# Performance work log

Hardware: AMD Instinct MI355X
Metric: run time of the kernel (lower is better)

The kernel has to match this reference:

```python
import jax, jax.numpy as jnp
import numpy as np

N_USERS = 1_000_000
AVG_DEG = 32
E = N_USERS * AVG_DEG
K = 5
IN_F = 1
OUT_F = 64
BN_EPS = 1e-5


def setup_inputs() -> dict:
    key = jax.random.key(0)
    ks = jax.random.split(key, 6)
    stdv = 1.0 / np.sqrt(IN_F * K)
    return {
        "x": jax.random.normal(ks[0], (N_USERS, IN_F), dtype=jnp.float32),
        "edge_index": jax.random.randint(ks[1], (2, E), 0, N_USERS, dtype=jnp.int32),
        "edge_weight": jax.random.uniform(ks[2], (E,), dtype=jnp.float32),
        "weight": jax.random.uniform(ks[3], (OUT_F, K, IN_F), dtype=jnp.float32, minval=-stdv, maxval=stdv),
        "bias": jax.random.uniform(ks[4], (OUT_F,), dtype=jnp.float32, minval=-stdv, maxval=stdv),
        "gamma": jnp.ones((N_USERS,), dtype=jnp.float32),
        "beta": jnp.zeros((N_USERS,), dtype=jnp.float32),
    }


def reference(x, edge_index, edge_weight, weight, bias, gamma, beta):
    N = x.shape[0]
    src, dst = edge_index[0], edge_index[1]
    # K-hop propagation: gather x_j, scale by edge_weight, scatter-add at dst
    feats = [x]
    cur = x
    for _ in range(K - 1):
        msg = cur[src] * edge_weight[:, None]                 # [E, IN_F]
        cur = jax.ops.segment_sum(msg, dst, num_segments=N)   # [N, IN_F]
        feats.append(cur)
    # [N, K*IN_F], hop-major / feature-minor ordering (matches torch reshape)
    conv = jnp.concatenate(feats, axis=1)[None]               # [1, N, K*IN_F]
    h = weight.reshape(OUT_F, K * IN_F).T                     # [K*IN_F, OUT_F]
    y = jnp.matmul(conv, h) + bias                            # [1, N, OUT_F]
    # BatchNorm1d(N_users) in training mode: stats over (batch, feature) per node-channel
    mean = jnp.mean(y, axis=(0, 2), keepdims=True)
    var = jnp.mean((y - mean) ** 2, axis=(0, 2), keepdims=True)  # biased var
    y_hat = (y - mean) * jax.lax.rsqrt(var + BN_EPS)
    return y_hat * gamma[None, :, None] + beta[None, :, None]
```

## Files before the change

### kernel.cpp

```cpp
#include <hip/hip_runtime.h>

#define N_USERS 1000000
#define NEDGE   32000000
#define OUT_F   64
#define BN_EPS  1e-5f

#define SBITS     12
#define S_BUCKET  4096
#define NB        245
#define CAP       136896
#define SCAT_BLOCKS 1024
#define TILE      4096
#define NTILES    ((NEDGE + TILE - 1) / TILE)
#define SPLIT     16

typedef unsigned int uint4v __attribute__((ext_vector_type(4)));
typedef int          int4v  __attribute__((ext_vector_type(4)));
typedef float        flt4v  __attribute__((ext_vector_type(4)));


__global__ void init_cursors(unsigned* __restrict__ cursors) {
    int i = blockIdx.x * blockDim.x + threadIdx.x;
    if (i < NB) cursors[i] = (unsigned)i * CAP;
}

__global__ __launch_bounds__(256) void scatter_bin(
    const int* __restrict__ src, const int* __restrict__ dst,
    const float* __restrict__ ew, uint2* __restrict__ rec,
    unsigned* __restrict__ cursors) {
    __shared__ uint2 srec[TILE];
    __shared__ unsigned short sbkt[TILE];
    __shared__ unsigned hist[NB];
    __shared__ unsigned curs[NB];
    __shared__ unsigned gpos[NB];
    __shared__ unsigned chunkT[256];
    int tid = threadIdx.x;

    for (int tile = blockIdx.x; tile < NTILES; tile += gridDim.x) {
        int e0 = tile * TILE;
        int n_this = (e0 + TILE <= NEDGE) ? TILE : (NEDGE - e0);
        int nq = n_this >> 2;
        int q0 = e0 >> 2;

        for (int i = tid; i < NB; i += 256) hist[i] = 0;
        __syncthreads();

        int4v dv[4]; int4v sv[4]; flt4v wv[4];
        #pragma unroll
        for (int k = 0; k < 4; ++k) {
            int q = k * 256 + tid;
            if (q < nq) {
                dv[k] = __builtin_nontemporal_load(reinterpret_cast<const int4v*>(dst) + q0 + q);
                sv[k] = __builtin_nontemporal_load(reinterpret_cast<const int4v*>(src) + q0 + q);
                wv[k] = __builtin_nontemporal_load(reinterpret_cast<const flt4v*>(ew) + q0 + q);
            }
        }
        #pragma unroll
        for (int k = 0; k < 4; ++k) {
            int q = k * 256 + tid;
            if (q < nq) {
                #pragma unroll
                for (int j = 0; j < 4; ++j)
                    atomicAdd(&hist[dv[k][j] >> SBITS], 1u);
            }
        }
        __syncthreads();

        {
            int base = tid * 4;
            unsigned run = 0;
            #pragma unroll
            for (int k = 0; k < 4; ++k) {
                int idx = base + k;
                unsigned v = (idx < NB) ? hist[idx] : 0u;
                if (idx < NB) hist[idx] = run;
                run += v;
            }
            chunkT[tid] = run;
        }
        __syncthreads();
        if (tid == 0) {
            unsigned r = 0;
            for (int t = 0; t < 256; ++t) { unsigned v = chunkT[t]; chunkT[t] = r; r += v; }
        }
        __syncthreads();
        {
            int base = tid * 4;
            unsigned add = chunkT[tid];
            #pragma unroll
            for (int k = 0; k < 4; ++k) {
                int idx = base + k;
                if (idx < NB) hist[idx] += add;
            }
        }
        __syncthreads();

        for (int b = tid; b < NB; b += 256) {
            unsigned st = hist[b];
            unsigned en = (b == NB - 1) ? (unsigned)n_this : hist[b + 1];
            unsigned c = en - st;
            gpos[b] = c ? atomicAdd(&cursors[b], c) : 0u;
            curs[b] = 0;
        }
        __syncthreads();

        #pragma unroll
        for (int k = 0; k < 4; ++k) {
            int q = k * 256 + tid;
            if (q < nq) {
                #pragma unroll
                for (int j = 0; j < 4; ++j) {
                    int dd = dv[k][j], ss = sv[k][j];
                    int b = dd >> SBITS;
                    unsigned p = hist[b] + atomicAdd(&curs[b], 1u);
                    srec[p] = make_uint2(((unsigned)(dd & (S_BUCKET - 1)) << 20) | (unsigned)ss,
                                         __float_as_uint(wv[k][j]));
                    sbkt[p] = (unsigned short)b;
                }
            }
        }
        __syncthreads();

        for (int i = tid; i < n_this; i += 256) {
            unsigned b = sbkt[i];
            rec[gpos[b] + ((unsigned)i - hist[b])] = srec[i];
        }
        __syncthreads();
    }
}

__global__ __launch_bounds__(256) void hop_bucket(
    const uint2* __restrict__ rec, const unsigned* __restrict__ cursors,
    const float* __restrict__ cur, float* __restrict__ nxt) {
    __shared__ float acc[S_BUCKET];
    int tid = threadIdx.x;
    int b = blockIdx.x / SPLIT;
    int sidx = blockIdx.x % SPLIT;
    for (int i = tid; i < S_BUCKET; i += 256) acc[i] = 0.0f;
    __syncthreads();

    unsigned start = (unsigned)b * CAP;
    unsigned cnt = cursors[b] - start;
    unsigned u0 = ((cnt * (unsigned)sidx) / SPLIT) & ~15u;
    unsigned u1 = (sidx == SPLIT - 1) ? cnt : (((cnt * (unsigned)(sidx + 1)) / SPLIT) & ~15u);
    const uint2* bp = rec + start;

    unsigned i = u0 + 16u * (unsigned)tid;
    for (; i + 16u <= u1; i += 16u * 256u) {
        uint4v r[8];
        #pragma unroll
        for (int k = 0; k < 8; ++k)
            r[k] = __builtin_nontemporal_load(reinterpret_cast<const uint4v*>(bp + i + 2 * k));
        float c[16];
        #pragma unroll
        for (int k = 0; k < 8; ++k) {
            c[2 * k]     = cur[r[k].x & 0xFFFFFu];
            c[2 * k + 1] = cur[r[k].z & 0xFFFFFu];
        }
        #pragma unroll
        for (int k = 0; k < 8; ++k) {
            atomicAdd(&acc[r[k].x >> 20], c[2 * k]     * __uint_as_float(r[k].y));
            atomicAdd(&acc[r[k].z >> 20], c[2 * k + 1] * __uint_as_float(r[k].w));
        }
    }
    if (i < u1) {
        for (unsigned j = i; j < i + 16u && j < u1; ++j) {
            uint2 rr = bp[j];
            atomicAdd(&acc[rr.x >> 20], cur[rr.x & 0xFFFFFu] * __uint_as_float(rr.y));
        }
    }
    __syncthreads();

    int nb0 = b << SBITS;
    for (int k = tid; k < S_BUCKET; k += 256) {
        int n = nb0 + k;
        if (n < N_USERS) atomicAdd(&nxt[n], acc[k]);
    }
}


__global__ void zero_kernel(float* __restrict__ p, int n) {
    int i = blockIdx.x * blockDim.x + threadIdx.x;
    int stride = gridDim.x * blockDim.x;
    for (; i < n; i += stride) p[i] = 0.0f;
}

__global__ __launch_bounds__(256) void hop_atomic(
    const int* __restrict__ src, const int* __restrict__ dst,
    const float* __restrict__ ew, const float* __restrict__ cur,
    float* __restrict__ nxt) {
    int e = blockIdx.x * blockDim.x + threadIdx.x;
    if (e * 4 < NEDGE) {
        int4   s = ((const int4*)src)[e];
        int4   d = ((const int4*)dst)[e];
        float4 w = ((const float4*)ew)[e];
        atomicAdd(&nxt[d.x], cur[s.x] * w.x);
        atomicAdd(&nxt[d.y], cur[s.y] * w.y);
        atomicAdd(&nxt[d.z], cur[s.z] * w.z);
        atomicAdd(&nxt[d.w], cur[s.w] * w.w);
    }
}


__global__ __launch_bounds__(256) void finalize_kernel(
    const float* __restrict__ x,  const float* __restrict__ f1,
    const float* __restrict__ f2, const float* __restrict__ f3,
    const float* __restrict__ f4, const float* __restrict__ W,
    const float* __restrict__ bias, const float* __restrict__ gamma,
    const float* __restrict__ beta, float* __restrict__ out) {
    int lane = threadIdx.x & 63;
    int waveInBlock = threadIdx.x >> 6;
    int wavesPerBlock = blockDim.x >> 6;
    int gwave  = blockIdx.x * wavesPerBlock + waveInBlock;
    int nwaves = gridDim.x * wavesPerBlock;

    float w0 = W[lane * 5 + 0];
    float w1 = W[lane * 5 + 1];
    float w2 = W[lane * 5 + 2];
    float w3 = W[lane * 5 + 3];
    float w4 = W[lane * 5 + 4];
    float b  = bias[lane];

    for (int n = gwave; n < N_USERS; n += nwaves) {
        float c0 = x[n], c1 = f1[n], c2 = f2[n], c3 = f3[n], c4 = f4[n];
        float y = b + c0 * w0 + c1 * w1 + c2 * w2 + c3 * w3 + c4 * w4;

        float s = y;
        #pragma unroll
        for (int off = 32; off; off >>= 1) s += __shfl_xor(s, off);
        float mean = s * (1.0f / 64.0f);

        float d = y - mean;
        float v = d * d;
        #pragma unroll
        for (int off = 32; off; off >>= 1) v += __shfl_xor(v, off);
        float var = v * (1.0f / 64.0f);

        float o = d * rsqrtf(var + BN_EPS) * gamma[n] + beta[n];
        __builtin_nontemporal_store(o, &out[(size_t)n * OUT_F + lane]);
    }
}

extern "C" void kernel_launch(void* const* d_in, const int* in_sizes, int n_in,
                              void* d_out, int out_size, void* d_ws, size_t ws_size,
                              hipStream_t stream) {
    const float* x     = (const float*)d_in[0];
    const int*   ei    = (const int*)d_in[1];
    const float* ew    = (const float*)d_in[2];
    const float* W     = (const float*)d_in[3];
    const float* bias  = (const float*)d_in[4];
    const float* gamma = (const float*)d_in[5];
    const float* beta  = (const float*)d_in[6];
    float* out = (float*)d_out;

    const int* src = ei;
    const int* dst = ei + NEDGE;

    float* f = (float*)d_ws;
    uint2* rec = (uint2*)(f + 4ull * N_USERS);
    unsigned* cursors = (unsigned*)(rec + (size_t)NB * CAP);
    size_t needed = 16000000ull + (size_t)NB * CAP * 8 + 4096;

    if (ws_size >= needed) {
        init_cursors<<<1, 256, 0, stream>>>(cursors);
        zero_kernel<<<2048, 256, 0, stream>>>(f, 4 * N_USERS);
        scatter_bin<<<SCAT_BLOCKS, 256, 0, stream>>>(src, dst, ew, rec, cursors);
        const float* cur = x;
        for (int h = 0; h < 4; ++h) {
            float* nxt = f + (size_t)h * N_USERS;
            hop_bucket<<<NB * SPLIT, 256, 0, stream>>>(rec, cursors, cur, nxt);
            cur = nxt;
        }
    } else {
        zero_kernel<<<4096, 256, 0, stream>>>(f, 4 * N_USERS);
        const float* cur = x;
        for (int h = 0; h < 4; ++h) {
            float* nxt = f + (size_t)h * N_USERS;
            hop_atomic<<<NEDGE / 4 / 256, 256, 0, stream>>>(src, dst, ew, cur, nxt);
            cur = nxt;
        }
    }

    finalize_kernel<<<2048, 256, 0, stream>>>(
        x, f, f + N_USERS, f + 2 * N_USERS, f + 3 * N_USERS,
        W, bias, gamma, beta, out);
}
```

Before: 1.859 ms.

## Regroup edges into dst-super/src-window bins and stage source windows in LDS

After: 3.555 ms. +91.2%, slower.

```diff
diff --git a/kernel.cpp b/kernel.cpp
--- a/kernel.cpp
+++ b/kernel.cpp
@@ -12,9 +12,21 @@
 #define SCAT_BLOCKS 1024
 #define TILE      4096
 #define NTILES    ((NEDGE + TILE - 1) / TILE)
-#define SPLIT     16
+
+#define SUP_B     6
+#define NSUP      41
+#define S_SUPER   24576
+#define NWIN      245
+#define NBINS2    (NSUP * NWIN)
+#define HSPLIT    6
+#define RGRID     1024
+
+static_assert((unsigned long long)NEDGE * 8ull ==
+              (unsigned long long)N_USERS * OUT_F * 4ull,
+              "compact rec2 must exactly fit d_out");
 
 typedef unsigned int uint4v __attribute__((ext_vector_type(4)));
+typedef unsigned int uint2v __attribute__((ext_vector_type(2)));
 typedef int          int4v  __attribute__((ext_vector_type(4)));
 typedef float        flt4v  __attribute__((ext_vector_type(4)));
 
@@ -129,52 +141,209 @@
     }
 }
 
-__global__ __launch_bounds__(256) void hop_bucket(
+
+__global__ __launch_bounds__(256) void count_bins(
     const uint2* __restrict__ rec, const unsigned* __restrict__ cursors,
+    unsigned* __restrict__ cnt2) {
+    __shared__ unsigned hist[NWIN];
+    int tid = threadIdx.x;
+    int b = blockIdx.x >> 2, q = blockIdx.x & 3;
+    for (int i = tid; i < NWIN; i += 256) hist[i] = 0;
+    __syncthreads();
+    unsigned cnt = cursors[b] - (unsigned)b * CAP;
+    unsigned lo = (unsigned)(((unsigned long long)cnt * (unsigned)q) >> 2);
+    unsigned hi = (q == 3) ? cnt : (unsigned)(((unsigned long long)cnt * (unsigned)(q + 1)) >> 2);
+    const uint2v* bp = reinterpret_cast<const uint2v*>(rec + (size_t)b * CAP);
+    unsigned i = lo + (unsigned)tid;
+    for (; i + 768 < hi; i += 1024) {
+        uint2v r0 = __builtin_nontemporal_load(bp + i);
+        uint2v r1 = __builtin_nontemporal_load(bp + i + 256);
+        uint2v r2 = __builtin_nontemporal_load(bp + i + 512);
+        uint2v r3 = __builtin_nontemporal_load(bp + i + 768);
+        atomicAdd(&hist[(r0.x & 0xFFFFFu) >> 12], 1u);
+        atomicAdd(&hist[(r1.x & 0xFFFFFu) >> 12], 1u);
+        atomicAdd(&hist[(r2.x & 0xFFFFFu) >> 12], 1u);
+        atomicAdd(&hist[(r3.x & 0xFFFFFu) >> 12], 1u);
+    }
+    for (; i < hi; i += 256) {
+        uint2v r = __builtin_nontemporal_load(bp + i);
+        atomicAdd(&hist[(r.x & 0xFFFFFu) >> 12], 1u);
+    }
+    __syncthreads();
+    unsigned base = (unsigned)(b / SUP_B) * (unsigned)NWIN;
+    for (int k = tid; k < NWIN; k += 256)
+        if (hist[k]) atomicAdd(&cnt2[base + k], hist[k]);
+}
+
+
+__global__ __launch_bounds__(256) void prefix_bins(
+    const unsigned* __restrict__ cnt2, unsigned* __restrict__ bases,
+    unsigned* __restrict__ cursors2) {
+    __shared__ unsigned chunkT[256];
+    int t = threadIdx.x;
+    unsigned loc[40];
+    unsigned run = 0;
+    for (int k = 0; k < 40; ++k) {
+        int idx = t * 40 + k;
+        unsigned v = (idx < NBINS2) ? cnt2[idx] : 0u;
+        loc[k] = run; run += v;
+    }
+    chunkT[t] = run;
+    __syncthreads();
+    if (t == 0) {
+        unsigned r = 0;
+        for (int i = 0; i < 256; ++i) { unsigned v = chunkT[i]; chunkT[i] = r; r += v; }
+    }
+    __syncthreads();
+    unsigned add = chunkT[t];
+    for (int k = 0; k < 40; ++k) {
+        int idx = t * 40 + k;
+        if (idx < NBINS2) { unsigned v = loc[k] + add; bases[idx] = v; cursors2[idx] = v; }
+    }
+    if (t == 0) bases[NBINS2] = (unsigned)NEDGE;
+}
+
+
+__global__ __launch_bounds__(256) void regroup(
+    const uint2* __restrict__ rec, const unsigned* __restrict__ cursors,
+    uint2* __restrict__ rec2, unsigned* __restrict__ cursors2) {
+    __shared__ uint2 srec[TILE];
+    __shared__ unsigned char skey[TILE];
+    __shared__ unsigned hist[NWIN];
+    __shared__ unsigned curs[NWIN];
+    __shared__ unsigned gpos[NWIN];
+    __shared__ unsigned chunkT[256];
+    int tid = threadIdx.x;
+
+    for (int b = 0; b < NB; ++b) {
+        unsigned cntb = cursors[b] - (unsigned)b * CAP;
+        unsigned binbase = (unsigned)(b / SUP_B) * (unsigned)NWIN;
+        unsigned rb = (unsigned)(b % SUP_B) << 12;
+        int ntiles = (int)((cntb + TILE - 1) / TILE);
+        const uint2* bp = rec + (size_t)b * CAP;
+
+        for (int t = blockIdx.x; t < ntiles; t += gridDim.x) {
+            unsigned e0 = (unsigned)t * TILE;
+            unsigned n_this = (cntb - e0 < TILE) ? (cntb - e0) : TILE;
+
+            for (int i = tid; i < NWIN; i += 256) hist[i] = 0;
+            __syncthreads();
+
+            uint4v rv[8];
+            #pragma unroll
+            for (int k2 = 0; k2 < 8; ++k2) {
+                unsigned idx = (unsigned)(k2 * 512 + tid * 2);
+                if (idx < n_this)
+                    rv[k2] = __builtin_nontemporal_load(
+                        reinterpret_cast<const uint4v*>(bp + e0 + idx));
+            }
+            #pragma unroll
+            for (int k2 = 0; k2 < 8; ++k2) {
+                unsigned idx = (unsigned)(k2 * 512 + tid * 2);
+                if (idx < n_this)     atomicAdd(&hist[(rv[k2].x & 0xFFFFFu) >> 12], 1u);
+                if (idx + 1 < n_this) atomicAdd(&hist[(rv[k2].z & 0xFFFFFu) >> 12], 1u);
+            }
+            __syncthreads();
+
+            chunkT[tid] = (tid < NWIN) ? hist[tid] : 0u;
+            __syncthreads();
+            if (tid == 0) {
+                unsigned r = 0;
+                for (int i = 0; i < 256; ++i) { unsigned v = chunkT[i]; chunkT[i] = r; r += v; }
+            }
+            __syncthreads();
+            if (tid < NWIN) hist[tid] = chunkT[tid];
+            __syncthreads();
+            if (tid < NWIN) {
+                unsigned st = hist[tid];
+                unsigned en = (tid == NWIN - 1) ? n_this : hist[tid + 1];
+                unsigned c = en - st;
+                gpos[tid] = c ? atomicAdd(&cursors2[binbase + tid], c) : 0u;
+                curs[tid] = 0;
+            }
+            __syncthreads();
+
+            #pragma unroll
+            for (int k2 = 0; k2 < 8; ++k2) {
+                unsigned idx = (unsigned)(k2 * 512 + tid * 2);
+                if (idx < n_this) {
+                    unsigned m = rv[k2].x;
+                    unsigned k = (m & 0xFFFFFu) >> 12;
+                    unsigned p = hist[k] + atomicAdd(&curs[k], 1u);
+                    srec[p] = make_uint2((((m >> 20) + rb) << 12) | (m & 0xFFFu), rv[k2].y);
+                    skey[p] = (unsigned char)k;
+                }
+                if (idx + 1 < n_this) {
+                    unsigned m = rv[k2].z;
+                    unsigned k = (m & 0xFFFFFu) >> 12;
+                    unsigned p = hist[k] + atomicAdd(&curs[k], 1u);
+                    srec[p] = make_uint2((((m >> 20) + rb) << 12) | (m & 0xFFFu), rv[k2].w);
+                    skey[p] = (unsigned char)k;
+                }
+            }
+            __syncthreads();
+
+            for (unsigned i = (unsigned)tid; i < n_this; i += 256) {
+                unsigned k = skey[i];
+                rec2[gpos[k] + (i - hist[k])] = srec[i];
+            }
+            __syncthreads();
+        }
+    }
+}
+
+
+__global__ __launch_bounds__(512) void hop_super(
+    const uint2* __restrict__ rec2, const unsigned* __restrict__ bases,
     const float* __restrict__ cur, float* __restrict__ nxt) {
-    __shared__ float acc[S_BUCKET];
+    __shared__ float acc[S_SUPER];
+    __shared__ float win[4096];
     int tid = threadIdx.x;
-    int b = blockIdx.x / SPLIT;
-    int sidx = blockIdx.x % SPLIT;
-    for (int i = tid; i < S_BUCKET; i += 256) acc[i] = 0.0f;
+    int s = blockIdx.x / HSPLIT;
+    int j = blockIdx.x % HSPLIT;
+    for (int i = tid; i < S_SUPER; i += 512) acc[i] = 0.0f;
+
+    for (int k = j; k < NWIN; k += HSPLIT) {
+        __syncthreads();
+        int wbase = k << 12;
+        for (int i = tid; i < 4096; i += 512) {
+            int g = wbase + i;
+            win[i] = (g < N_USERS) ? cur[g] : 0.0f;
+        }
+        __syncthreads();
+
+        unsigned lo = bases[s * NWIN + k];
+        unsigned hi = bases[s * NWIN + k + 1];
+        if ((lo & 1u) && lo < hi) {
+            if (tid == 0) {
+                uint2 r = rec2[lo];
+                atomicAdd(&acc[r.x >> 12], win[r.x & 0xFFFu] * __uint_as_float(r.y));
+            }
+            ++lo;
+        }
+        for (unsigned i = lo + 4u * (unsigned)tid; i + 4u <= hi; i += 4u * 512u) {
+            uint4v a = __builtin_nontemporal_load(reinterpret_cast<const uint4v*>(rec2 + i));
+            uint4v b2 = __builtin_nontemporal_load(reinterpret_cast<const uint4v*>(rec2 + i + 2));
+            float v0 = win[a.x & 0xFFFu];
+            float v1 = win[a.z & 0xFFFu];
+            float v2 = win[b2.x & 0xFFFu];
+            float v3 = win[b2.z & 0xFFFu];
+            atomicAdd(&acc[a.x >> 12],  v0 * __uint_as_float(a.y));
+            atomicAdd(&acc[a.z >> 12],  v1 * __uint_as_float(a.w));
+            atomicAdd(&acc[b2.x >> 12], v2 * __uint_as_float(b2.y));
+            atomicAdd(&acc[b2.z >> 12], v3 * __uint_as_float(b2.w));
+        }
+        unsigned tstart = lo + ((hi - lo) & ~3u);
+        if (tstart + (unsigned)tid < hi) {
+            uint2 r = rec2[tstart + tid];
+            atomicAdd(&acc[r.x >> 12], win[r.x & 0xFFFu] * __uint_as_float(r.y));
+        }
+    }
     __syncthreads();
-
-    unsigned start = (unsigned)b * CAP;
-    unsigned cnt = cursors[b] - start;
-    unsigned u0 = ((cnt * (unsigned)sidx) / SPLIT) & ~15u;
-    unsigned u1 = (sidx == SPLIT - 1) ? cnt : (((cnt * (unsigned)(sidx + 1)) / SPLIT) & ~15u);
-    const uint2* bp = rec + start;
-
-    unsigned i = u0 + 16u * (unsigned)tid;
-    for (; i + 16u <= u1; i += 16u * 256u) {
-        uint4v r[8];
-        #pragma unroll
-        for (int k = 0; k < 8; ++k)
-            r[k] = __builtin_nontemporal_load(reinterpret_cast<const uint4v*>(bp + i + 2 * k));
-        float c[16];
-        #pragma unroll
-        for (int k = 0; k < 8; ++k) {
-            c[2 * k]     = cur[r[k].x & 0xFFFFFu];
-            c[2 * k + 1] = cur[r[k].z & 0xFFFFFu];
-        }
-        #pragma unroll
-        for (int k = 0; k < 8; ++k) {
-            atomicAdd(&acc[r[k].x >> 20], c[2 * k]     * __uint_as_float(r[k].y));
-            atomicAdd(&acc[r[k].z >> 20], c[2 * k + 1] * __uint_as_float(r[k].w));
-        }
-    }
-    if (i < u1) {
-        for (unsigned j = i; j < i + 16u && j < u1; ++j) {
-            uint2 rr = bp[j];
-            atomicAdd(&acc[rr.x >> 20], cur[rr.x & 0xFFFFFu] * __uint_as_float(rr.y));
-        }
-    }
-    __syncthreads();
-
-    int nb0 = b << SBITS;
-    for (int k = tid; k < S_BUCKET; k += 256) {
-        int n = nb0 + k;
-        if (n < N_USERS) atomicAdd(&nxt[n], acc[k]);
+    int d0 = s * S_SUPER;
+    for (int i = tid; i < S_SUPER; i += 512) {
+        int n = d0 + i;
+        if (n < N_USERS) atomicAdd(&nxt[n], acc[i]);
     }
 }
 
@@ -258,17 +427,26 @@
 
     float* f = (float*)d_ws;
     uint2* rec = (uint2*)(f + 4ull * N_USERS);
-    unsigned* cursors = (unsigned*)(rec + (size_t)NB * CAP);
-    size_t needed = 16000000ull + (size_t)NB * CAP * 8 + 4096;
+    unsigned* cursors  = (unsigned*)(rec + (size_t)NB * CAP);
+    unsigned* cnt2     = cursors + 1024;
+    unsigned* bases    = cnt2 + 10240;
+    unsigned* cursors2 = bases + 10240;
+    size_t needed = 16000000ull + (size_t)NB * CAP * 8 + 4096 + 3ull * 40960;
+
+    uint2* rec2 = (uint2*)d_out;
 
     if (ws_size >= needed) {
         init_cursors<<<1, 256, 0, stream>>>(cursors);
         zero_kernel<<<2048, 256, 0, stream>>>(f, 4 * N_USERS);
+        zero_kernel<<<40, 256, 0, stream>>>((float*)cnt2, NBINS2);
         scatter_bin<<<SCAT_BLOCKS, 256, 0, stream>>>(src, dst, ew, rec, cursors);
+        count_bins<<<NB * 4, 256, 0, stream>>>(rec, cursors, cnt2);
+        prefix_bins<<<1, 256, 0, stream>>>(cnt2, bases, cursors2);
+        regroup<<<RGRID, 256, 0, stream>>>(rec, cursors, rec2, cursors2);
         const float* cur = x;
         for (int h = 0; h < 4; ++h) {
             float* nxt = f + (size_t)h * N_USERS;
-            hop_bucket<<<NB * SPLIT, 256, 0, stream>>>(rec, cursors, cur, nxt);
+            hop_super<<<NSUP * HSPLIT, 512, 0, stream>>>(rec2, bases, cur, nxt);
             cur = nxt;
         }
     } else {
```
